# Kernel optimization log

Measured on AMD Instinct MI355X. Metric: run time of the kernel, lower is better.

Reference implementation:

```python
import jax, jax.numpy as jnp
import numpy as np

B, S, E = 2, 2048, 1024
H = 16
D = E // H
LAYER_IDX = 2.0
MASKED_BIAS = -10000.0


def setup_inputs() -> dict:
    key = jax.random.key(0)
    k1, k2, k3 = jax.random.split(key, 3)
    hidden_state = jax.random.normal(k1, (B, S, E), dtype=jnp.float32)
    w_attn = jax.random.normal(k2, (E, 3 * E), dtype=jnp.float32) * 0.2
    b_attn = jnp.zeros((3 * E,), dtype=jnp.float32)
    w_proj = jax.random.normal(k3, (E, E), dtype=jnp.float32) * 0.2
    b_proj = jnp.zeros((E,), dtype=jnp.float32)
    return {"hidden_state": hidden_state, "w_attn": w_attn, "b_attn": b_attn,
            "w_proj": w_proj, "b_proj": b_proj}


def reference(hidden_state, w_attn, b_attn, w_proj, b_proj):
    b, s, e = hidden_state.shape
    # c_attn: Conv1D == x @ W + b, then split into q, k, v
    qkv = hidden_state @ w_attn + b_attn          # [b, s, 3E]
    q, k, v = jnp.split(qkv, 3, axis=-1)
    # split heads -> [b, H, s, D]
    def split_heads(t):
        return t.reshape(b, s, H, D).transpose(0, 2, 1, 3)
    q, k, v = split_heads(q), split_heads(k), split_heads(v)
    # QK^T scaled by sqrt(d_head) then by layer_idx
    scores = jnp.einsum("bhqd,bhkd->bhqk", q, k)
    scores = scores / jnp.asarray(D ** 0.5, scores.dtype)
    scores = scores / LAYER_IDX
    # causal mask with masked_bias fill (-10000.0), matching bias buffer slice
    causal = jnp.tril(jnp.ones((s, s), dtype=bool))  # [s, s]
    scores = jnp.where(causal[None, None, :, :], scores, jnp.asarray(MASKED_BIAS, scores.dtype))
    attn = jax.nn.softmax(scores, axis=-1)
    out = jnp.einsum("bhqk,bhkd->bhqd", attn, v)   # [b, H, s, D]
    # merge heads
    out = out.transpose(0, 2, 1, 3).reshape(b, s, e)
    # c_proj
    return out @ w_proj + b_proj
```

## Files before the change

### kernel.cpp

```cpp
#include <hip/hip_runtime.h>
#include <cstddef>
#include <cstdint>

#define B_DIM   2
#define S_LEN   2048
#define EMB     1024
#define NH      16
#define HD      64
#define QKV_N   3072
#define MROWS   (B_DIM * S_LEN)

using half8  = __attribute__((ext_vector_type(8))) _Float16;
using half4  = __attribute__((ext_vector_type(4))) _Float16;
using f32x4  = __attribute__((ext_vector_type(4))) float;

#if defined(__has_builtin)
#if __has_builtin(__builtin_amdgcn_global_load_lds)
#define HAS_GLL 1
#endif
#endif

__device__ __forceinline__ void stage16(const _Float16* g, _Float16* lds_base, int lane)
{
#ifdef HAS_GLL
    (void)lane;
    __builtin_amdgcn_global_load_lds(
        (const __attribute__((address_space(1))) unsigned int*)g,
        (__attribute__((address_space(3))) unsigned int*)lds_base, 16, 0, 0);
#else
    *(half8*)(lds_base + lane * 8) = *(const half8*)g;
#endif
}

__global__ __launch_bounds__(256)
void prep_all(const float* __restrict__ hidden, const float* __restrict__ w_attn,
              const float* __restrict__ w_proj, _Float16* __restrict__ hidden_h,
              _Float16* __restrict__ wattn_t, _Float16* __restrict__ wproj_t)
{
    const int bid = blockIdx.x, t = threadIdx.x;
    if (bid < 4096) {
        int i = bid * 1024 + t * 4;
        float4 v = *(const float4*)(hidden + i);
        half4 h = { (_Float16)v.x, (_Float16)v.y, (_Float16)v.z, (_Float16)v.w };
        *(half4*)(hidden_h + i) = h;
        return;
    }
    __shared__ float T[32][33];
    const float* W; _Float16* Wt; int N, bx, by;
    if (bid < 7168) {
        int t2 = bid - 4096; bx = t2 % 96; by = t2 / 96; W = w_attn; Wt = wattn_t; N = QKV_N;
    } else {
        int t3 = bid - 7168; bx = t3 & 31; by = t3 >> 5; W = w_proj; Wt = wproj_t; N = EMB;
    }
    const int n0 = bx * 32, k0 = by * 32;
    const int r = t >> 3, c4 = (t & 7) * 4;
    float4 w = *(const float4*)(W + (size_t)(k0 + r) * N + n0 + c4);
    T[r][c4 + 0] = w.x; T[r][c4 + 1] = w.y;
    T[r][c4 + 2] = w.z; T[r][c4 + 3] = w.w;
    __syncthreads();
    half4 h = { (_Float16)T[c4 + 0][r], (_Float16)T[c4 + 1][r],
                (_Float16)T[c4 + 2][r], (_Float16)T[c4 + 3][r] };
    *(half4*)(Wt + (size_t)(n0 + r) * EMB + k0 + c4) = h;
}

template <int MT, int MINW, bool OUT_F16, bool FUSE_VT>
__global__ __launch_bounds__(256, MINW)
void hgemm_lds(const _Float16* __restrict__ X, const _Float16* __restrict__ Wt,
               const float* __restrict__ bias, void* __restrict__ Cout,
               _Float16* __restrict__ vt, int M, int N, int K)
{
    constexpr int BM = MT * 32;
    constexpr int ACALLS = BM / 32;
    __shared__ _Float16 As[BM][64];
    __shared__ _Float16 Bs[128][64];

    const int tid  = threadIdx.x;
    const int wave = tid >> 6, lane = tid & 63;
    const int quad = lane >> 4, l15 = lane & 15;
    const int wm = (wave >> 1) * (MT * 16);
    const int wn = (wave & 1) * 64;
    const int m0 = blockIdx.y * BM, n0 = blockIdx.x * 128;

    const int srow = lane >> 3;
    const int scol = ((lane & 7) ^ srow) * 8;

    const _Float16* xg[ACALLS];
#pragma unroll
    for (int c = 0; c < ACALLS; ++c)
        xg[c] = X + (size_t)(m0 + wave * (BM / 4) + c * 8 + srow) * K + scol;
    const _Float16* wg[4];
#pragma unroll
    for (int c = 0; c < 4; ++c)
        wg[c] = Wt + (size_t)(n0 + wave * 32 + c * 8 + srow) * K + scol;

    f32x4 acc[MT][4] = {};
    const int sx = l15 & 7;

    for (int k0 = 0; k0 < K; k0 += 64) {
#pragma unroll
        for (int c = 0; c < ACALLS; ++c)
            stage16(xg[c] + k0, &As[wave * (BM / 4) + c * 8][0], lane);
#pragma unroll
        for (int c = 0; c < 4; ++c)
            stage16(wg[c] + k0, &Bs[wave * 32 + c * 8][0], lane);
        __syncthreads();

#pragma unroll
        for (int cc = 0; cc < 2; ++cc) {
            half8 af[MT], bf[4];
#pragma unroll
            for (int mt = 0; mt < MT; ++mt)
                af[mt] = *(const half8*)&As[wm + mt * 16 + l15][(((cc * 4 + quad) ^ sx)) * 8];
#pragma unroll
            for (int nt = 0; nt < 4; ++nt)
                bf[nt] = *(const half8*)&Bs[wn + nt * 16 + l15][(((cc * 4 + quad) ^ sx)) * 8];
#pragma unroll
            for (int mt = 0; mt < MT; ++mt)
#pragma unroll
                for (int nt = 0; nt < 4; ++nt)
                    acc[mt][nt] = __builtin_amdgcn_mfma_f32_16x16x32_f16(
                        af[mt], bf[nt], acc[mt][nt], 0, 0, 0);
        }
        __syncthreads();
    }

    if (FUSE_VT && n0 >= 2 * EMB) {
#pragma unroll
        for (int nt = 0; nt < 4; ++nt) {
            const int c  = n0 + wn + nt * 16 + l15;
            const float bv = bias[c];
            const int vcol = c - 2 * EMB;
            const int hh = vcol >> 6, dd = vcol & 63;
#pragma unroll
            for (int mt = 0; mt < MT; ++mt) {
                const int r = m0 + wm + mt * 16 + quad * 4;
                const int bb = r >> 11, ss = r & 2047;
                half4 o = { (_Float16)(acc[mt][nt][0] + bv), (_Float16)(acc[mt][nt][1] + bv),
                            (_Float16)(acc[mt][nt][2] + bv), (_Float16)(acc[mt][nt][3] + bv) };
                *(half4*)(vt + ((size_t)(bb * NH + hh) * HD + dd) * S_LEN + ss) = o;
            }
        }
        return;
    }

#pragma unroll
    for (int nt = 0; nt < 4; ++nt) {
        const int c = n0 + wn + nt * 16 + l15;
        const float bv = bias[c];
#pragma unroll
        for (int mt = 0; mt < MT; ++mt)
#pragma unroll
            for (int reg = 0; reg < 4; ++reg) {
                const int r = m0 + wm + mt * 16 + quad * 4 + reg;
                const float v = acc[mt][nt][reg] + bv;
                if (OUT_F16)
                    ((_Float16*)Cout)[(size_t)r * N + c] = (_Float16)v;
                else
                    ((float*)Cout)[(size_t)r * N + c] = v;
            }
    }
}

__global__ __launch_bounds__(256, 4)
void attn_fa_mfma6(const _Float16* __restrict__ qkv,
                   const _Float16* __restrict__ vt,
                   _Float16* __restrict__ outh)
{
    __shared__ _Float16 Ks[128][64];
    __shared__ _Float16 Vs[64][128];

    const int n   = blockIdx.x;
    const int xcd = n & 7, g = (n >> 3) & 3, j = n >> 5;
    const int bh  = xcd * 4 + g;
    const int qt  = (j < 16) ? j : (47 - j);
    const int b = bh >> 4, h = bh & 15;

    const int tid  = threadIdx.x;
    const int wave = tid >> 6, lane = tid & 63;
    const int quad = lane >> 4, l15 = lane & 15;
    const size_t row0 = (size_t)b * S_LEN;

    const _Float16 qscale = (_Float16)0.0901684400555602f;
    half8 qf[2];
    {
        const size_t qrow = row0 + qt * 64 + wave * 16 + l15;
        const _Float16* qp = qkv + qrow * QKV_N + h * HD + quad * 8;
#pragma unroll
        for (int c = 0; c < 2; ++c) {
            half8 q = *(const half8*)(qp + c * 32);
#pragma unroll
            for (int j2 = 0; j2 < 8; ++j2) q[j2] = q[j2] * qscale;
            qf[c] = q;
        }
    }

    f32x4 o_acc[4] = {};
    float m_i = -1e30f, l_i = 0.0f;

    const int ksrow = lane >> 3;
    const int kscol = ((lane & 7) ^ ksrow) * 8;
    const int vsrow = lane >> 4;
    const _Float16* vbase = vt + (size_t)bh * HD * S_LEN;
    const int sxk = l15 & 7;

    const int ktN = (qt + 2) >> 1;
    for (int kt = 0; kt < ktN; ++kt) {
        __syncthreads();
        {
            const _Float16* kbase = qkv + (row0 + kt * 128) * QKV_N + EMB + h * HD;
#pragma unroll
            for (int c = 0; c < 4; ++c) {
                const int r0 = wave * 32 + c * 8;
                stage16(kbase + (size_t)(r0 + ksrow) * QKV_N + kscol,
                        &Ks[r0][0], lane);
            }
#pragma unroll
            for (int c = 0; c < 4; ++c) {
                const int r0 = wave * 16 + c * 4;
                const int sgv = ((lane & 15) ^ (c * 4 + vsrow)) * 8;
                stage16(vbase + (size_t)(r0 + vsrow) * S_LEN + kt * 128 + sgv,
                        &Vs[r0][0], lane);
            }
        }
        __syncthreads();

        f32x4 st[8] = {};
#pragma unroll
        for (int c = 0; c < 2; ++c)
#pragma unroll
            for (int nt = 0; nt < 8; ++nt) {
                half8 kf = *(const half8*)&Ks[nt * 16 + l15][((c * 4 + quad) ^ sxk) * 8];
                st[nt] = __builtin_amdgcn_mfma_f32_16x16x32_f16(kf, qf[c], st[nt], 0, 0, 0);
            }

        if (kt == ktN - 1) {
            const int q = qt * 64 + wave * 16 + l15;
#pragma unroll
            for (int nt = 0; nt < 8; ++nt) {
                const int ks = kt * 128 + nt * 16 + quad * 4;
#pragma unroll
                for (int reg = 0; reg < 4; ++reg)
                    if (ks + reg > q) st[nt][reg] = -1e30f;
            }
        }

        float rm = fmaxf(fmaxf(st[0][0], st[0][1]), fmaxf(st[0][2], st[0][3]));
#pragma unroll
        for (int nt = 1; nt < 8; ++nt) {
            rm = fmaxf(rm, fmaxf(st[nt][0], st[nt][1]));
            rm = fmaxf(rm, fmaxf(st[nt][2], st[nt][3]));
        }
        rm = fmaxf(rm, __shfl_xor(rm, 16));
        rm = fmaxf(rm, __shfl_xor(rm, 32));
        const float mnew = fmaxf(m_i, rm);

        if (__ballot(mnew > m_i)) {
            const float alpha = __builtin_amdgcn_exp2f(m_i - mnew);
            l_i *= alpha;
#pragma unroll
            for (int dt = 0; dt < 4; ++dt)
#pragma unroll
                for (int reg = 0; reg < 4; ++reg) o_acc[dt][reg] *= alpha;
        }
        m_i = mnew;

        float rs = 0.0f;
        half4 pf[8];
#pragma unroll
        for (int nt = 0; nt < 8; ++nt) {
            float p0 = __builtin_amdgcn_exp2f(st[nt][0] - mnew);
            float p1 = __builtin_amdgcn_exp2f(st[nt][1] - mnew);
            float p2 = __builtin_amdgcn_exp2f(st[nt][2] - mnew);
            float p3 = __builtin_amdgcn_exp2f(st[nt][3] - mnew);
            rs += (p0 + p1) + (p2 + p3);
            pf[nt] = half4{ (_Float16)p0, (_Float16)p1, (_Float16)p2, (_Float16)p3 };
        }
        rs += __shfl_xor(rs, 16);
        rs += __shfl_xor(rs, 32);
        l_i += rs;

#pragma unroll
        for (int nt = 0; nt < 8; ++nt)
#pragma unroll
            for (int dt = 0; dt < 4; ++dt) {
                const int pg = ((2 * nt + (quad >> 1)) ^ l15) * 8 + (quad & 1) * 4;
                half4 vf = *(const half4*)&Vs[dt * 16 + l15][pg];
                o_acc[dt] = __builtin_amdgcn_mfma_f32_16x16x16f16(vf, pf[nt], o_acc[dt], 0, 0, 0);
            }
    }

    const float inv = 1.0f / l_i;
    const size_t r = row0 + qt * 64 + wave * 16 + l15;
#pragma unroll
    for (int dt = 0; dt < 4; ++dt) {
        half4 o = { (_Float16)(o_acc[dt][0] * inv), (_Float16)(o_acc[dt][1] * inv),
                    (_Float16)(o_acc[dt][2] * inv), (_Float16)(o_acc[dt][3] * inv) };
        *(half4*)(outh + r * EMB + h * HD + dt * 16 + quad * 4) = o;
    }
}

extern "C" void kernel_launch(void* const* d_in, const int* in_sizes, int n_in,
                              void* d_out, int out_size, void* d_ws, size_t ws_size,
                              hipStream_t stream)
{
    const float* hidden = (const float*)d_in[0];
    const float* w_attn = (const float*)d_in[1];
    const float* b_attn = (const float*)d_in[2];
    const float* w_proj = (const float*)d_in[3];
    const float* b_proj = (const float*)d_in[4];

    _Float16* hidden_h = (_Float16*)d_ws;
    _Float16* wattn_t  = hidden_h + (size_t)MROWS * EMB;
    _Float16* wproj_t  = wattn_t + (size_t)EMB * QKV_N;
    _Float16* qkv_h    = wproj_t + (size_t)EMB * EMB;
    _Float16* attn_h   = qkv_h + (size_t)MROWS * QKV_N;
    _Float16* vt       = attn_h + (size_t)MROWS * EMB;

    prep_all<<<8192, 256, 0, stream>>>(hidden, w_attn, w_proj,
                                       hidden_h, wattn_t, wproj_t);

    hgemm_lds<4, 3, true, true><<<dim3(QKV_N / 128, MROWS / 128), 256, 0, stream>>>(
        hidden_h, wattn_t, b_attn, qkv_h, vt, MROWS, QKV_N, EMB);

    attn_fa_mfma6<<<dim3(1024), 256, 0, stream>>>(qkv_h, vt, attn_h);

    hgemm_lds<2, 4, false, false><<<dim3(EMB / 128, MROWS / 64), 256, 0, stream>>>(
        attn_h, wproj_t, b_proj, d_out, nullptr, MROWS, EMB, EMB);
}
```

Measured before the change: 183.7 us.

## Process paired causal query tiles per block to share K/V staging

Each attention block now handles two query tiles (j and 31-j) of the same head, so every K/V tile staged into LDS serves both tiles while they overlap, and the work per block is balanced across the causal triangle. Grid size is halved and launch bounds drop to 2 blocks per CU, which allows more registers for the doubled accumulators and score tiles. This cuts repeated global-to-LDS K/V loads and syncs, but lowers occupancy and raises register pressure.

```diff
diff --git a/kernel.cpp b/kernel.cpp
--- a/kernel.cpp
+++ b/kernel.cpp
@@ -161,8 +161,8 @@
     }
 }
 
-__global__ __launch_bounds__(256, 4)
-void attn_fa_mfma6(const _Float16* __restrict__ qkv,
+__global__ __launch_bounds__(256, 2)
+void attn_fa_mfma7(const _Float16* __restrict__ qkv,
                    const _Float16* __restrict__ vt,
                    _Float16* __restrict__ outh)
 {
@@ -172,7 +172,7 @@
     const int n   = blockIdx.x;
     const int xcd = n & 7, g = (n >> 3) & 3, j = n >> 5;
     const int bh  = xcd * 4 + g;
-    const int qt  = (j < 16) ? j : (47 - j);
+    const int qta = j, qtb = 31 - j;
     const int b = bh >> 4, h = bh & 15;
 
     const int tid  = threadIdx.x;
@@ -181,21 +181,22 @@
     const size_t row0 = (size_t)b * S_LEN;
 
     const _Float16 qscale = (_Float16)0.0901684400555602f;
-    half8 qf[2];
+    half8 qfa[2], qfb[2];
     {
-        const size_t qrow = row0 + qt * 64 + wave * 16 + l15;
-        const _Float16* qp = qkv + qrow * QKV_N + h * HD + quad * 8;
+        const _Float16* qpa = qkv + (row0 + qta * 64 + wave * 16 + l15) * QKV_N + h * HD + quad * 8;
+        const _Float16* qpb = qkv + (row0 + qtb * 64 + wave * 16 + l15) * QKV_N + h * HD + quad * 8;
 #pragma unroll
         for (int c = 0; c < 2; ++c) {
-            half8 q = *(const half8*)(qp + c * 32);
-#pragma unroll
-            for (int j2 = 0; j2 < 8; ++j2) q[j2] = q[j2] * qscale;
-            qf[c] = q;
-        }
-    }
-
-    f32x4 o_acc[4] = {};
-    float m_i = -1e30f, l_i = 0.0f;
+            half8 qa = *(const half8*)(qpa + c * 32);
+            half8 qb = *(const half8*)(qpb + c * 32);
+#pragma unroll
+            for (int j2 = 0; j2 < 8; ++j2) { qa[j2] *= qscale; qb[j2] *= qscale; }
+            qfa[c] = qa; qfb[c] = qb;
+        }
+    }
+
+    f32x4 o_a[4] = {}, o_b[4] = {};
+    float m_a = -1e30f, l_a = 0.0f, m_b = -1e30f, l_b = 0.0f;
 
     const int ksrow = lane >> 3;
     const int kscol = ((lane & 7) ^ ksrow) * 8;
@@ -203,47 +204,8 @@
     const _Float16* vbase = vt + (size_t)bh * HD * S_LEN;
     const int sxk = l15 & 7;
 
-    const int ktN = (qt + 2) >> 1;
-    for (int kt = 0; kt < ktN; ++kt) {
-        __syncthreads();
-        {
-            const _Float16* kbase = qkv + (row0 + kt * 128) * QKV_N + EMB + h * HD;
-#pragma unroll
-            for (int c = 0; c < 4; ++c) {
-                const int r0 = wave * 32 + c * 8;
-                stage16(kbase + (size_t)(r0 + ksrow) * QKV_N + kscol,
-                        &Ks[r0][0], lane);
-            }
-#pragma unroll
-            for (int c = 0; c < 4; ++c) {
-                const int r0 = wave * 16 + c * 4;
-                const int sgv = ((lane & 15) ^ (c * 4 + vsrow)) * 8;
-                stage16(vbase + (size_t)(r0 + vsrow) * S_LEN + kt * 128 + sgv,
-                        &Vs[r0][0], lane);
-            }
-        }
-        __syncthreads();
-
-        f32x4 st[8] = {};
-#pragma unroll
-        for (int c = 0; c < 2; ++c)
-#pragma unroll
-            for (int nt = 0; nt < 8; ++nt) {
-                half8 kf = *(const half8*)&Ks[nt * 16 + l15][((c * 4 + quad) ^ sxk) * 8];
-                st[nt] = __builtin_amdgcn_mfma_f32_16x16x32_f16(kf, qf[c], st[nt], 0, 0, 0);
-            }
-
-        if (kt == ktN - 1) {
-            const int q = qt * 64 + wave * 16 + l15;
-#pragma unroll
-            for (int nt = 0; nt < 8; ++nt) {
-                const int ks = kt * 128 + nt * 16 + quad * 4;
-#pragma unroll
-                for (int reg = 0; reg < 4; ++reg)
-                    if (ks + reg > q) st[nt][reg] = -1e30f;
-            }
-        }
-
+    auto softmax_pack = [&](f32x4 (&st)[8], half4 (&pf)[8], float& m_i, float& l_i,
+                            f32x4 (&o_acc)[4]) {
         float rm = fmaxf(fmaxf(st[0][0], st[0][1]), fmaxf(st[0][2], st[0][3]));
 #pragma unroll
         for (int nt = 1; nt < 8; ++nt) {
@@ -253,7 +215,6 @@
         rm = fmaxf(rm, __shfl_xor(rm, 16));
         rm = fmaxf(rm, __shfl_xor(rm, 32));
         const float mnew = fmaxf(m_i, rm);
-
         if (__ballot(mnew > m_i)) {
             const float alpha = __builtin_amdgcn_exp2f(m_i - mnew);
             l_i *= alpha;
@@ -263,9 +224,7 @@
                 for (int reg = 0; reg < 4; ++reg) o_acc[dt][reg] *= alpha;
         }
         m_i = mnew;
-
         float rs = 0.0f;
-        half4 pf[8];
 #pragma unroll
         for (int nt = 0; nt < 8; ++nt) {
             float p0 = __builtin_amdgcn_exp2f(st[nt][0] - mnew);
@@ -278,24 +237,112 @@
         rs += __shfl_xor(rs, 16);
         rs += __shfl_xor(rs, 32);
         l_i += rs;
-
-#pragma unroll
-        for (int nt = 0; nt < 8; ++nt)
-#pragma unroll
-            for (int dt = 0; dt < 4; ++dt) {
-                const int pg = ((2 * nt + (quad >> 1)) ^ l15) * 8 + (quad & 1) * 4;
-                half4 vf = *(const half4*)&Vs[dt * 16 + l15][pg];
-                o_acc[dt] = __builtin_amdgcn_mfma_f32_16x16x16f16(vf, pf[nt], o_acc[dt], 0, 0, 0);
-            }
-    }
-
-    const float inv = 1.0f / l_i;
-    const size_t r = row0 + qt * 64 + wave * 16 + l15;
-#pragma unroll
-    for (int dt = 0; dt < 4; ++dt) {
-        half4 o = { (_Float16)(o_acc[dt][0] * inv), (_Float16)(o_acc[dt][1] * inv),
-                    (_Float16)(o_acc[dt][2] * inv), (_Float16)(o_acc[dt][3] * inv) };
-        *(half4*)(outh + r * EMB + h * HD + dt * 16 + quad * 4) = o;
+    };
+
+    const int ktNa = (qta + 2) >> 1;
+    const int ktNb = (qtb + 2) >> 1;
+
+    for (int kt = 0; kt < ktNb; ++kt) {
+        __syncthreads();
+        {
+            const _Float16* kbase = qkv + (row0 + kt * 128) * QKV_N + EMB + h * HD;
+#pragma unroll
+            for (int c = 0; c < 4; ++c) {
+                const int r0 = wave * 32 + c * 8;
+                stage16(kbase + (size_t)(r0 + ksrow) * QKV_N + kscol, &Ks[r0][0], lane);
+            }
+#pragma unroll
+            for (int c = 0; c < 4; ++c) {
+                const int r0 = wave * 16 + c * 4;
+                const int sgv = ((lane & 15) ^ (c * 4 + vsrow)) * 8;
+                stage16(vbase + (size_t)(r0 + vsrow) * S_LEN + kt * 128 + sgv, &Vs[r0][0], lane);
+            }
+        }
+        __syncthreads();
+
+        if (kt < ktNa) {
+            f32x4 sa[8] = {}, sb[8] = {};
+#pragma unroll
+            for (int c = 0; c < 2; ++c)
+#pragma unroll
+                for (int nt = 0; nt < 8; ++nt) {
+                    half8 kf = *(const half8*)&Ks[nt * 16 + l15][((c * 4 + quad) ^ sxk) * 8];
+                    sa[nt] = __builtin_amdgcn_mfma_f32_16x16x32_f16(kf, qfa[c], sa[nt], 0, 0, 0);
+                    sb[nt] = __builtin_amdgcn_mfma_f32_16x16x32_f16(kf, qfb[c], sb[nt], 0, 0, 0);
+                }
+            if (kt == ktNa - 1) {
+                const int q = qta * 64 + wave * 16 + l15;
+#pragma unroll
+                for (int nt = 0; nt < 8; ++nt) {
+                    const int ks = kt * 128 + nt * 16 + quad * 4;
+#pragma unroll
+                    for (int reg = 0; reg < 4; ++reg)
+                        if (ks + reg > q) sa[nt][reg] = -1e30f;
+                }
+            }
+            half4 pfa[8], pfb[8];
+            softmax_pack(sa, pfa, m_a, l_a, o_a);
+            softmax_pack(sb, pfb, m_b, l_b, o_b);
+#pragma unroll
+            for (int nt = 0; nt < 8; ++nt)
+#pragma unroll
+                for (int dt = 0; dt < 4; ++dt) {
+                    const int pg = ((2 * nt + (quad >> 1)) ^ l15) * 8 + (quad & 1) * 4;
+                    half4 vf = *(const half4*)&Vs[dt * 16 + l15][pg];
+                    o_a[dt] = __builtin_amdgcn_mfma_f32_16x16x16f16(vf, pfa[nt], o_a[dt], 0, 0, 0);
+                    o_b[dt] = __builtin_amdgcn_mfma_f32_16x16x16f16(vf, pfb[nt], o_b[dt], 0, 0, 0);
+                }
+        } else {
+            f32x4 sb[8] = {};
+#pragma unroll
+            for (int c = 0; c < 2; ++c)
+#pragma unroll
+                for (int nt = 0; nt < 8; ++nt) {
+                    half8 kf = *(const half8*)&Ks[nt * 16 + l15][((c * 4 + quad) ^ sxk) * 8];
+                    sb[nt] = __builtin_amdgcn_mfma_f32_16x16x32_f16(kf, qfb[c], sb[nt], 0, 0, 0);
+                }
+            if (kt == ktNb - 1) {
+                const int q = qtb * 64 + wave * 16 + l15;
+#pragma unroll
+                for (int nt = 0; nt < 8; ++nt) {
+                    const int ks = kt * 128 + nt * 16 + quad * 4;
+#pragma unroll
+                    for (int reg = 0; reg < 4; ++reg)
+                        if (ks + reg > q) sb[nt][reg] = -1e30f;
+                }
+            }
+            half4 pfb[8];
+            softmax_pack(sb, pfb, m_b, l_b, o_b);
+#pragma unroll
+            for (int nt = 0; nt < 8; ++nt)
+#pragma unroll
+                for (int dt = 0; dt < 4; ++dt) {
+                    const int pg = ((2 * nt + (quad >> 1)) ^ l15) * 8 + (quad & 1) * 4;
+                    half4 vf = *(const half4*)&Vs[dt * 16 + l15][pg];
+                    o_b[dt] = __builtin_amdgcn_mfma_f32_16x16x16f16(vf, pfb[nt], o_b[dt], 0, 0, 0);
+                }
+        }
+    }
+
+    {
+        const float inv = 1.0f / l_a;
+        const size_t r = row0 + qta * 64 + wave * 16 + l15;
+#pragma unroll
+        for (int dt = 0; dt < 4; ++dt) {
+            half4 o = { (_Float16)(o_a[dt][0] * inv), (_Float16)(o_a[dt][1] * inv),
+                        (_Float16)(o_a[dt][2] * inv), (_Float16)(o_a[dt][3] * inv) };
+            *(half4*)(outh + r * EMB + h * HD + dt * 16 + quad * 4) = o;
+        }
+    }
+    {
+        const float inv = 1.0f / l_b;
+        const size_t r = row0 + qtb * 64 + wave * 16 + l15;
+#pragma unroll
+        for (int dt = 0; dt < 4; ++dt) {
+            half4 o = { (_Float16)(o_b[dt][0] * inv), (_Float16)(o_b[dt][1] * inv),
+                        (_Float16)(o_b[dt][2] * inv), (_Float16)(o_b[dt][3] * inv) };
+            *(half4*)(outh + r * EMB + h * HD + dt * 16 + quad * 4) = o;
+        }
     }
 }
 
@@ -322,7 +369,7 @@
     hgemm_lds<4, 3, true, true><<<dim3(QKV_N / 128, MROWS / 128), 256, 0, stream>>>(
         hidden_h, wattn_t, b_attn, qkv_h, vt, MROWS, QKV_N, EMB);
 
-    attn_fa_mfma6<<<dim3(1024), 256, 0, stream>>>(qkv_h, vt, attn_h);
+    attn_fa_mfma7<<<dim3(512), 256, 0, stream>>>(qkv_h, vt, attn_h);
 
     hgemm_lds<2, 4, false, false><<<dim3(EMB / 128, MROWS / 64), 256, 0, stream>>>(
         attn_h, wproj_t, b_proj, d_out, nullptr, MROWS, EMB, EMB);
```

New measurement: 172.7 us. -6.0%, faster.
